# Optimization experiments

Measured on AMD Instinct MI355X. Metric: run time of the kernel, lower is better.

Reference implementation:

```python
import jax, jax.numpy as jnp
import numpy as np

NUM_HEADS = 8
WS = 7          # window size (hardcoded in source)
SR = 4          # sr_ratio
EPS = 1e-5


def _win_partition(t, ws, H, W):
    # t: [B, h, N, d] -> [B*h*nW, ws*ws, d]
    B, h, N, d = t.shape
    t = t.reshape(B * h, H // ws, ws, W // ws, ws, d)
    t = t.transpose(0, 1, 3, 2, 4, 5)
    return t.reshape(-1, ws * ws, d)


def _win_reverse(w, ws, H, W, h):
    # w: [B*h*nW, ws*ws, d] -> [B, H*W, h*d]
    d = w.shape[-1]
    Bh = w.shape[0] // ((H // ws) * (W // ws))
    x = w.reshape(Bh, H // ws, W // ws, ws, ws, d).transpose(0, 1, 3, 2, 4, 5)
    x = x.reshape(Bh // h, h, H, W, d).transpose(0, 2, 3, 1, 4)
    return x.reshape(Bh // h, H * W, h * d)


def setup_inputs() -> dict:
    key = jax.random.key(0)
    B, H, W, C = 32, 56, 56, 256
    N = H * W
    ks = jax.random.split(key, 10)
    s = lambda k, shp: jax.random.normal(k, shp, dtype=jnp.float32) * 0.02
    return {
        "x": jax.random.normal(ks[0], (B, N, C), dtype=jnp.float32),
        "lepe_lin_w": s(ks[1], (C, C)), "lepe_lin_b": jnp.zeros((C,), jnp.float32),
        "lepe_conv_w": s(ks[2], (3, 3, 1, C)), "lepe_conv_b": jnp.zeros((C,), jnp.float32),
        "sr_w": s(ks[3], (SR, SR, C, C)), "sr_b": jnp.zeros((C,), jnp.float32),
        "norm_g": jnp.ones((C,), jnp.float32), "norm_b": jnp.zeros((C,), jnp.float32),
        "q1_w": s(ks[4], (C, C // 2)), "kv1_w": s(ks[5], (C, C)),
        "q2_w": s(ks[6], (C, C // 2)), "kv2_w": s(ks[7], (C, C)),
        "proj_w": s(ks[8], (C, C)), "proj_b": jnp.zeros((C,), jnp.float32),
        "H": H, "W": W,
    }


def reference(x, lepe_lin_w, lepe_lin_b, lepe_conv_w, lepe_conv_b, sr_w, sr_b,
              norm_g, norm_b, q1_w, kv1_w, q2_w, kv2_w, proj_w, proj_b, H, W):
    B, N, C = x.shape
    h2 = NUM_HEADS // 2
    d = C // NUM_HEADS
    scale = d ** (-0.5)

    # lepe: linear -> depthwise 3x3 conv (NHWC) -> flatten back
    lep = (x @ lepe_lin_w + lepe_lin_b).reshape(B, H, W, C)
    lep = jax.lax.conv_general_dilated(
        lep, lepe_conv_w, window_strides=(1, 1), padding='SAME',
        dimension_numbers=('NHWC', 'HWIO', 'NHWC'), feature_group_count=C) + lepe_conv_b
    lepe = lep.reshape(B, N, C)

    # --- branch 1: global attention over sr-downsampled kv ---
    q1 = (x @ q1_w).reshape(B, N, h2, d).transpose(0, 2, 1, 3)         # [B,h2,N,d]
    img = x.reshape(B, H, W, C)
    x1_ = jax.lax.conv_general_dilated(
        img, sr_w, window_strides=(SR, SR), padding='VALID',
        dimension_numbers=('NHWC', 'HWIO', 'NHWC')) + sr_b              # [B,H/sr,W/sr,C]
    x1_ = x1_.reshape(B, -1, C)                                         # [B,N1,C]
    mu = jnp.mean(x1_, axis=-1, keepdims=True)
    var = jnp.mean(jnp.square(x1_ - mu), axis=-1, keepdims=True)
    x1_ = (x1_ - mu) * jax.lax.rsqrt(var + EPS) * norm_g + norm_b
    x1_ = jax.nn.gelu(x1_, approximate=False)
    kv1 = (x1_ @ kv1_w).reshape(B, -1, 2, h2, d).transpose(2, 0, 3, 1, 4)
    k1, v1 = kv1[0], kv1[1]                                             # [B,h2,N1,d]
    attn1 = jax.nn.softmax(jnp.einsum('bhnd,bhmd->bhnm', q1, k1) * scale, axis=-1)
    x1 = jnp.einsum('bhnm,bhmd->bhnd', attn1, v1)
    x1 = x1.transpose(0, 2, 1, 3).reshape(B, N, C // 2)

    # --- branch 2: 7x7 window attention ---
    q2 = (x @ q2_w).reshape(B, N, h2, d).transpose(0, 2, 1, 3)          # [B,h2,N,d]
    kv2 = (x @ kv2_w).reshape(B, -1, 2, h2, d).transpose(2, 0, 3, 1, 4)
    k2, v2 = kv2[0], kv2[1]
    q2w = _win_partition(q2, WS, H, W)                                  # [B*h2*nW,49,d]
    k2w = _win_partition(k2, WS, H, W)
    v2w = _win_partition(v2, WS, H, W)
    attn2 = jax.nn.softmax(jnp.einsum('wnd,wmd->wnm', q2w, k2w) * scale, axis=-1)
    x2w = jnp.einsum('wnm,wmd->wnd', attn2, v2w)
    x2 = _win_reverse(x2w, WS, H, W, h2)                                # [B,N,C/2]

    out = jnp.concatenate([x1, x2], axis=-1)
    out = (out + lepe) @ proj_w + proj_b
    return out
```

## Files before the change

kernel.cpp:

```cpp
#include <hip/hip_runtime.h>
#include <hip/hip_bf16.h>

typedef __hip_bfloat16 bf16;
typedef __attribute__((ext_vector_type(8))) short short8;
typedef __attribute__((ext_vector_type(4))) float floatx4;

__device__ __forceinline__ float toF(bf16 v){ return __bfloat162float(v); }
__device__ __forceinline__ float b2f(unsigned short u){
  return __uint_as_float(((unsigned int)u) << 16);
}
__device__ __forceinline__ unsigned short f2bu(float f){
  bf16 h = __float2bfloat16(f);
  return *(unsigned short*)&h;
}
__device__ __forceinline__ void storeT(bf16* p, float v){ *p = __float2bfloat16(v); }
__device__ __forceinline__ void storeT(float* p, float v){ *p = v; }

__device__ __forceinline__ void gl2l16(const void* g, void* l) {
  __builtin_amdgcn_global_load_lds(
      (const __attribute__((address_space(1))) unsigned int*)g,
      (__attribute__((address_space(3))) unsigned int*)l, 16, 0, 0);
}

__global__ __launch_bounds__(256) void cvt_x_kernel(
    const float* __restrict__ in, bf16* __restrict__ out) {
  size_t i4 = ((size_t)blockIdx.x * 256 + threadIdx.x) * 4;
  float4 v = *(const float4*)(in + i4);
  ushort4 o;
  o.x = f2bu(v.x); o.y = f2bu(v.y); o.z = f2bu(v.z); o.w = f2bu(v.w);
  *(ushort4*)(out + i4) = o;
}

__global__ __launch_bounds__(256) void prep_kernel(
    const float* __restrict__ sr_w, const float* __restrict__ lepe_w,
    const float* __restrict__ kv2_w, const float* __restrict__ q1_w,
    const float* __restrict__ q2_w, const float* __restrict__ kv1_w,
    const float* __restrict__ proj_w,
    bf16* __restrict__ wT_sr, bf16* __restrict__ wT_x,
    bf16* __restrict__ wT_kv1, bf16* __restrict__ wT_proj,
    int* __restrict__ srbase) {
  const int bid = blockIdx.x, tid = threadIdx.x;
  const float* src; bf16* dst; int K, N, idx;
  if (bid < 4096)      { src = sr_w;   dst = wT_sr;          K = 4096; N = 256; idx = bid * 256 + tid; }
  else if (bid < 4352) { src = lepe_w; dst = wT_x;           K = 256;  N = 256; idx = (bid - 4096) * 256 + tid; }
  else if (bid < 4608) { src = kv2_w;  dst = wT_x + 65536;   K = 256;  N = 256; idx = (bid - 4352) * 256 + tid; }
  else if (bid < 4736) { src = q1_w;   dst = wT_x + 131072;  K = 256;  N = 128; idx = (bid - 4608) * 256 + tid; }
  else if (bid < 4864) { src = q2_w;   dst = wT_x + 163840;  K = 256;  N = 128; idx = (bid - 4736) * 256 + tid; }
  else if (bid < 5120) { src = kv1_w;  dst = wT_kv1;         K = 256;  N = 256; idx = (bid - 4864) * 256 + tid; }
  else if (bid < 5376) { src = proj_w; dst = wT_proj;        K = 256;  N = 256; idx = (bid - 5120) * 256 + tid; }
  else {
    int t = (bid - 5376) * 256 + tid;
    if (t < 6272) {
      int b = t / 196, p = t - b * 196;
      int oy = p / 14, ox = p - oy * 14;
      srbase[t] = ((b * 56 + oy * 4) * 56 + ox * 4) * 256;
    }
    return;
  }
  int k = idx / N, n = idx - k * N;
  dst[(size_t)n * K + k] = __float2bfloat16(src[idx]);
}

template<typename OT>
__global__ __launch_bounds__(256) void gemm_mfma(
    const bf16* __restrict__ A, const bf16* __restrict__ BT,
    const float* __restrict__ bias, OT* __restrict__ C,
    int M, int K, int N) {
  __shared__ bf16 As[128 * 32];
  __shared__ bf16 Bs[128 * 32];
  const int tid = threadIdx.x;
  const int m0 = blockIdx.y * 128;
  const int n0 = blockIdx.x * 128;
  const int wave = tid >> 6, lane = tid & 63;
  const int wm = (wave >> 1) * 64, wn = (wave & 1) * 64;
  const int l15 = lane & 15, quad = lane >> 4;
  const int srow = lane >> 2, sseg = lane & 3;
  floatx4 zero = {0.f, 0.f, 0.f, 0.f};
  floatx4 acc[4][4];
#pragma unroll
  for (int i = 0; i < 4; i++)
#pragma unroll
    for (int j = 0; j < 4; j++) acc[i][j] = zero;

  for (int k0 = 0; k0 < K; k0 += 32) {
#pragma unroll
    for (int t = 0; t < 2; t++) {
      int rb = wave * 32 + t * 16;
      int r = rb + srow;
      gl2l16(A + (size_t)(m0 + r) * K + k0 + sseg * 8, &As[rb * 32]);
      gl2l16(BT + (size_t)(n0 + r) * K + k0 + sseg * 8, &Bs[rb * 32]);
    }
    __syncthreads();
    short8 af[4], bfr[4];
#pragma unroll
    for (int i = 0; i < 4; i++)
      af[i] = *(const short8*)&As[(wm + i * 16 + l15) * 32 + quad * 8];
#pragma unroll
    for (int j = 0; j < 4; j++)
      bfr[j] = *(const short8*)&Bs[(wn + j * 16 + l15) * 32 + quad * 8];
#pragma unroll
    for (int i = 0; i < 4; i++)
#pragma unroll
      for (int j = 0; j < 4; j++)
        acc[i][j] = __builtin_amdgcn_mfma_f32_16x16x32_bf16(af[i], bfr[j], acc[i][j], 0, 0, 0);
    __syncthreads();
  }
#pragma unroll
  for (int j = 0; j < 4; j++) {
    int n = n0 + wn + j * 16 + l15;
    float bv = bias ? bias[n] : 0.0f;
#pragma unroll
    for (int i = 0; i < 4; i++) {
      int m = m0 + wm + i * 16 + quad * 4;
#pragma unroll
      for (int r = 0; r < 4; r++)
        storeT(&C[(size_t)(m + r) * N + n], acc[i][j][r] + bv);
    }
  }
}

__global__ __launch_bounds__(256) void gemm_x3(
    const bf16* __restrict__ A, const bf16* __restrict__ BT,
    const float* __restrict__ lepe_b,
    bf16* __restrict__ L1, bf16* __restrict__ KV2, bf16* __restrict__ Q12) {
  __shared__ bf16 As[128 * 32];
  __shared__ bf16 Bs[128 * 32];
  const int sw = (blockIdx.x & 7) * 588 + (blockIdx.x >> 3);
  const int bx = sw % 6, by = sw / 6;
  const int m0 = by * 128;
  const int n0 = bx * 128;
  const int tid = threadIdx.x;
  const int wave = tid >> 6, lane = tid & 63;
  const int wm = (wave >> 1) * 64, wn = (wave & 1) * 64;
  const int l15 = lane & 15, quad = lane >> 4;
  const int srow = lane >> 2, sseg = lane & 3;
  floatx4 zero = {0.f, 0.f, 0.f, 0.f};
  floatx4 acc[4][4];
#pragma unroll
  for (int i = 0; i < 4; i++)
#pragma unroll
    for (int j = 0; j < 4; j++) acc[i][j] = zero;

  for (int k0 = 0; k0 < 256; k0 += 32) {
#pragma unroll
    for (int t = 0; t < 2; t++) {
      int rb = wave * 32 + t * 16;
      int r = rb + srow;
      gl2l16(A + (size_t)(m0 + r) * 256 + k0 + sseg * 8, &As[rb * 32]);
      gl2l16(BT + (size_t)(n0 + r) * 256 + k0 + sseg * 8, &Bs[rb * 32]);
    }
    __syncthreads();
    short8 af[4], bfr[4];
#pragma unroll
    for (int i = 0; i < 4; i++)
      af[i] = *(const short8*)&As[(wm + i * 16 + l15) * 32 + quad * 8];
#pragma unroll
    for (int j = 0; j < 4; j++)
      bfr[j] = *(const short8*)&Bs[(wn + j * 16 + l15) * 32 + quad * 8];
#pragma unroll
    for (int i = 0; i < 4; i++)
#pragma unroll
      for (int j = 0; j < 4; j++)
        acc[i][j] = __builtin_amdgcn_mfma_f32_16x16x32_bf16(af[i], bfr[j], acc[i][j], 0, 0, 0);
    __syncthreads();
  }
  const int segN = n0 >> 8;
  bf16* Cd = (segN == 0) ? L1 : (segN == 1) ? KV2 : Q12;
  const int nc0 = n0 & 255;
#pragma unroll
  for (int j = 0; j < 4; j++) {
    int nl = nc0 + wn + j * 16 + l15;
    float bv = (segN == 0) ? lepe_b[nl] : 0.0f;
#pragma unroll
    for (int i = 0; i < 4; i++) {
      int m = m0 + wm + i * 16 + quad * 4;
#pragma unroll
      for (int r = 0; r < 4; r++)
        Cd[(size_t)(m + r) * 256 + nl] = __float2bfloat16(acc[i][j][r] + bv);
    }
  }
}

__global__ __launch_bounds__(256) void gemm_sr(
    const bf16* __restrict__ X, const bf16* __restrict__ BT,
    const int* __restrict__ base, float* __restrict__ C) {
  __shared__ bf16 As[128 * 32];
  __shared__ bf16 Bs[128 * 32];
  const int tid = threadIdx.x;
  const int m0 = blockIdx.y * 128;
  const int n0 = blockIdx.x * 128;
  const int kz = blockIdx.z;
  const int wave = tid >> 6, lane = tid & 63;
  const int wm = (wave >> 1) * 64, wn = (wave & 1) * 64;
  const int l15 = lane & 15, quad = lane >> 4;
  const int srow = lane >> 2, sseg = lane & 3;
  const int mb0 = base[m0 + wave * 32 + srow];
  const int mb1 = base[m0 + wave * 32 + 16 + srow];
  floatx4 zero = {0.f, 0.f, 0.f, 0.f};
  floatx4 acc[4][4];
#pragma unroll
  for (int i = 0; i < 4; i++)
#pragma unroll
    for (int j = 0; j < 4; j++) acc[i][j] = zero;

  const int kbeg = kz * 512;
  for (int k0 = kbeg; k0 < kbeg + 512; k0 += 32) {
    int k = k0 + sseg * 8;
    int kp = k >> 8, c = k & 255;
    int off = ((kp >> 2) * 56 + (kp & 3)) * 256 + c;
#pragma unroll
    for (int t = 0; t < 2; t++) {
      int rb = wave * 32 + t * 16;
      gl2l16(X + (size_t)(t ? mb1 : mb0) + off, &As[rb * 32]);
      gl2l16(BT + (size_t)(n0 + rb + srow) * 4096 + k, &Bs[rb * 32]);
    }
    __syncthreads();
    short8 af[4], bfr[4];
#pragma unroll
    for (int i = 0; i < 4; i++)
      af[i] = *(const short8*)&As[(wm + i * 16 + l15) * 32 + quad * 8];
#pragma unroll
    for (int j = 0; j < 4; j++)
      bfr[j] = *(const short8*)&Bs[(wn + j * 16 + l15) * 32 + quad * 8];
#pragma unroll
    for (int i = 0; i < 4; i++)
#pragma unroll
      for (int j = 0; j < 4; j++)
        acc[i][j] = __builtin_amdgcn_mfma_f32_16x16x32_bf16(af[i], bfr[j], acc[i][j], 0, 0, 0);
    __syncthreads();
  }
  float* Cp = C + (size_t)kz * (6272 * 256);
#pragma unroll
  for (int j = 0; j < 4; j++) {
    int n = n0 + wn + j * 16 + l15;
#pragma unroll
    for (int i = 0; i < 4; i++) {
      int m = m0 + wm + i * 16 + quad * 4;
#pragma unroll
      for (int r = 0; r < 4; r++)
        Cp[(size_t)(m + r) * 256 + n] = acc[i][j][r];
    }
  }
}

__global__ __launch_bounds__(256) void gemm_proj_mfma(
    const bf16* __restrict__ X1, const bf16* __restrict__ X2,
    const bf16* __restrict__ L2, const bf16* __restrict__ BT,
    const float* __restrict__ bias, float* __restrict__ C) {
  __shared__ uint4 As[128 * 5];
  __shared__ bf16 Bs[128 * 32];
  const int sw = (blockIdx.x & 7) * 196 + (blockIdx.x >> 3);
  const int tid = threadIdx.x;
  const int m0 = (sw >> 1) * 128;
  const int n0 = (sw & 1) * 128;
  const int wave = tid >> 6, lane = tid & 63;
  const int wm = (wave >> 1) * 64, wn = (wave & 1) * 64;
  const int l15 = lane & 15, quad = lane >> 4;
  const int srow = lane >> 2, sseg = lane & 3;
  floatx4 zero = {0.f, 0.f, 0.f, 0.f};
  floatx4 acc[4][4];
#pragma unroll
  for (int i = 0; i < 4; i++)
#pragma unroll
    for (int j = 0; j < 4; j++) acc[i][j] = zero;

  for (int k0 = 0; k0 < 256; k0 += 32) {
#pragma unroll
    for (int t = 0; t < 2; t++) {
      int rb = wave * 32 + t * 16;
      gl2l16(BT + (size_t)(n0 + rb + srow) * 256 + k0 + sseg * 8, &Bs[rb * 32]);
    }
#pragma unroll
    for (int it = 0; it < 2; it++) {
      int id = it * 256 + tid;
      int row = id >> 2, seg = id & 3;
      int k = k0 + seg * 8;
      int mrow = m0 + row;
      const bf16* src = (k < 128) ? X1 + (size_t)mrow * 128 + k
                                  : X2 + (size_t)mrow * 128 + (k - 128);
      uint4 va = *(const uint4*)src;
      uint4 vl = *(const uint4*)(L2 + (size_t)mrow * 256 + k);
      const unsigned short* pa = (const unsigned short*)&va;
      const unsigned short* pl = (const unsigned short*)&vl;
      unsigned short ov[8];
#pragma unroll
      for (int e = 0; e < 8; e++) ov[e] = f2bu(b2f(pa[e]) + b2f(pl[e]));
      As[row * 5 + seg] = *(const uint4*)ov;
    }
    __syncthreads();
    short8 af[4], bfr[4];
#pragma unroll
    for (int i = 0; i < 4; i++)
      af[i] = *(const short8*)&As[(wm + i * 16 + l15) * 5 + quad];
#pragma unroll
    for (int j = 0; j < 4; j++)
      bfr[j] = *(const short8*)&Bs[(wn + j * 16 + l15) * 32 + quad * 8];
#pragma unroll
    for (int i = 0; i < 4; i++)
#pragma unroll
      for (int j = 0; j < 4; j++)
        acc[i][j] = __builtin_amdgcn_mfma_f32_16x16x32_bf16(af[i], bfr[j], acc[i][j], 0, 0, 0);
    __syncthreads();
  }
#pragma unroll
  for (int j = 0; j < 4; j++) {
    int n = n0 + wn + j * 16 + l15;
    float bv = bias[n];
#pragma unroll
    for (int i = 0; i < 4; i++) {
      int m = m0 + wm + i * 16 + quad * 4;
#pragma unroll
      for (int r = 0; r < 4; r++)
        C[(size_t)(m + r) * 256 + n] = acc[i][j][r] + bv;
    }
  }
}

__global__ __launch_bounds__(256) void dwconv8_kernel(
    const bf16* __restrict__ in, const float* __restrict__ w,
    const float* __restrict__ bias, bf16* __restrict__ out) {
  const int idx = blockIdx.x * 256 + threadIdx.x;
  const int c8 = (idx & 31) * 8;
  const int sp = idx >> 5;
  const int xx = sp % 56;
  const int yb = sp / 56;
  const int yy = yb % 56;
  const int b  = yb / 56;
  float4 bb0 = *(const float4*)&bias[c8];
  float4 bb1 = *(const float4*)&bias[c8 + 4];
  float acc[8] = {bb0.x, bb0.y, bb0.z, bb0.w, bb1.x, bb1.y, bb1.z, bb1.w};
#pragma unroll
  for (int dy = 0; dy < 3; dy++) {
    int y = yy + dy - 1;
    if ((unsigned)y >= 56u) continue;
#pragma unroll
    for (int dx = 0; dx < 3; dx++) {
      int x = xx + dx - 1;
      if ((unsigned)x >= 56u) continue;
      uint4 v = *(const uint4*)&in[((size_t)((b * 56 + y) * 56 + x)) * 256 + c8];
      const unsigned short* pv = (const unsigned short*)&v;
      float4 w0 = *(const float4*)&w[(dy * 3 + dx) * 256 + c8];
      float4 w1 = *(const float4*)&w[(dy * 3 + dx) * 256 + c8 + 4];
      float wf[8] = {w0.x, w0.y, w0.z, w0.w, w1.x, w1.y, w1.z, w1.w};
#pragma unroll
      for (int e = 0; e < 8; e++) acc[e] += b2f(pv[e]) * wf[e];
    }
  }
  unsigned short o[8];
#pragma unroll
  for (int e = 0; e < 8; e++) o[e] = f2bu(acc[e]);
  *(uint4*)&out[(size_t)sp * 256 + c8] = *(const uint4*)o;
}

__global__ __launch_bounds__(256) void ln_gelu_kernel(
    const float* __restrict__ in, const float* __restrict__ srb,
    const float* __restrict__ g, const float* __restrict__ bb,
    bf16* __restrict__ out) {
  const int tok = blockIdx.x;
  const int tid = threadIdx.x;
  float v = srb[tid];
  const float* p = in + (size_t)tok * 256 + tid;
#pragma unroll
  for (int c = 0; c < 8; c++) v += p[(size_t)c * 1605632];
  float s = v, s2 = v * v;
#pragma unroll
  for (int o = 32; o > 0; o >>= 1) {
    s += __shfl_down(s, o, 64);
    s2 += __shfl_down(s2, o, 64);
  }
  __shared__ float rs[4], rs2[4];
  int wid = tid >> 6, lane = tid & 63;
  if (lane == 0) { rs[wid] = s; rs2[wid] = s2; }
  __syncthreads();
  float tot = rs[0] + rs[1] + rs[2] + rs[3];
  float tot2 = rs2[0] + rs2[1] + rs2[2] + rs2[3];
  float mean = tot * (1.0f / 256.0f);
  float var = tot2 * (1.0f / 256.0f) - mean * mean;
  float y = (v - mean) * rsqrtf(var + 1e-5f) * g[tid] + bb[tid];
  out[(size_t)tok * 256 + tid] =
      __float2bfloat16(0.5f * y * (1.0f + erff(y * 0.70710678118654752f)));
}

__global__ __launch_bounds__(256) void attn1_mfma(
    const bf16* __restrict__ Q12, const float* __restrict__ KV,
    bf16* __restrict__ O) {
  __shared__ bf16 sk[224 * 32];
  __shared__ bf16 svT[32 * 232];
  __shared__ bf16 pbuf[4][64 * 32];
  const int b = blockIdx.z, h = blockIdx.y, chunk = blockIdx.x;
  const int tid = threadIdx.x;
  const int wave = tid >> 6, lane = tid & 63;
  const int l15 = lane & 15, quad = lane >> 4;
  for (int i = tid; i < 224 * 8; i += 256) {
    int m = i >> 3, c = i & 7;
    float4 kf = {0.f, 0.f, 0.f, 0.f}, vf = {0.f, 0.f, 0.f, 0.f};
    if (m < 196) {
      const float* p = KV + ((size_t)(b * 196 + m)) * 256 + h * 32 + c * 4;
      kf = *(const float4*)p;
      vf = *(const float4*)(p + 128);
    }
    ushort4 ko;
    ko.x = f2bu(kf.x); ko.y = f2bu(kf.y); ko.z = f2bu(kf.z); ko.w = f2bu(kf.w);
    *(ushort4*)&sk[m * 32 + c * 4] = ko;
    svT[(c * 4 + 0) * 232 + m] = __float2bfloat16(vf.x);
    svT[(c * 4 + 1) * 232 + m] = __float2bfloat16(vf.y);
    svT[(c * 4 + 2) * 232 + m] = __float2bfloat16(vf.z);
    svT[(c * 4 + 3) * 232 + m] = __float2bfloat16(vf.w);
  }
  __syncthreads();
  const int q0 = chunk * 256 + wave * 64;
  short8 aq[4];
#pragma unroll
  for (int i = 0; i < 4; i++) {
    int qr = q0 + i * 16 + l15; if (qr > 3135) qr = 3135;
    aq[i] = *(const short8*)(Q12 + ((size_t)(b * 3136 + qr)) * 256 + h * 32 + quad * 8);
  }
  const float scale = 0.17677669529663687f;
  floatx4 zero = {0.f, 0.f, 0.f, 0.f};
  floatx4 acc[4][2];
  float lsum[4][4];
#pragma unroll
  for (int i = 0; i < 4; i++) {
    acc[i][0] = zero; acc[i][1] = zero;
#pragma unroll
    for (int r = 0; r < 4; r++) lsum[i][r] = 0.f;
  }
  bf16* pw = pbuf[wave];
  for (int c = 0; c < 7; c++) {
    const int kv0 = c * 32;
    short8 bk[2];
#pragma unroll
    for (int n = 0; n < 2; n++)
      bk[n] = *(const short8*)&sk[(kv0 + n * 16 + l15) * 32 + quad * 8];
    floatx4 s[4][2];
#pragma unroll
    for (int i = 0; i < 4; i++)
#pragma unroll
      for (int n = 0; n < 2; n++)
        s[i][n] = __builtin_amdgcn_mfma_f32_16x16x32_bf16(aq[i], bk[n], zero, 0, 0, 0);
#pragma unroll
    for (int i = 0; i < 4; i++)
#pragma unroll
      for (int n = 0; n < 2; n++) {
        bool valid = (kv0 + n * 16 + l15) < 196;
#pragma unroll
        for (int r = 0; r < 4; r++) {
          float p = valid ? __expf(s[i][n][r] * scale) : 0.f;
          lsum[i][r] += p;
          pw[(i * 16 + quad * 4 + r) * 32 + n * 16 + l15] = __float2bfloat16(p);
        }
      }
    asm volatile("s_waitcnt lgkmcnt(0)" ::: "memory");
    short8 ap[4], bv[2];
#pragma unroll
    for (int i = 0; i < 4; i++)
      ap[i] = *(const short8*)&pw[(i * 16 + l15) * 32 + quad * 8];
#pragma unroll
    for (int n = 0; n < 2; n++)
      bv[n] = *(const short8*)&svT[(n * 16 + l15) * 232 + kv0 + quad * 8];
#pragma unroll
    for (int i = 0; i < 4; i++)
#pragma unroll
      for (int n = 0; n < 2; n++)
        acc[i][n] = __builtin_amdgcn_mfma_f32_16x16x32_bf16(ap[i], bv[n], acc[i][n], 0, 0, 0);
  }
#pragma unroll
  for (int i = 0; i < 4; i++)
#pragma unroll
    for (int r = 0; r < 4; r++) {
      float v = lsum[i][r];
      v += __shfl_xor(v, 1, 64);
      v += __shfl_xor(v, 2, 64);
      v += __shfl_xor(v, 4, 64);
      v += __shfl_xor(v, 8, 64);
      lsum[i][r] = 1.0f / v;
    }
#pragma unroll
  for (int i = 0; i < 4; i++)
#pragma unroll
    for (int r = 0; r < 4; r++) {
      int qr = q0 + i * 16 + quad * 4 + r;
      if (qr < 3136) {
        bf16* op = O + ((size_t)(b * 3136 + qr)) * 128 + h * 32;
        op[l15]      = __float2bfloat16(acc[i][0][r] * lsum[i][r]);
        op[16 + l15] = __float2bfloat16(acc[i][1][r] * lsum[i][r]);
      }
    }
}

__global__ __launch_bounds__(256) void attn2_mfma(
    const bf16* __restrict__ Q12, const bf16* __restrict__ KV2,
    bf16* __restrict__ O) {
  __shared__ bf16 sk[64 * 136];
  __shared__ bf16 pb[4][64 * 72];
  const int b = blockIdx.y;
  const int win = blockIdx.x;
  const int wy = win >> 3, wx = win & 7;
  const int tid = threadIdx.x;
  const int wave = tid >> 6, lane = tid & 63;
  const int l15 = lane & 15, quad = lane >> 4;
  const int h = wave;

  for (int i = tid; i < 49 * 16; i += 256) {
    int m = i >> 4, c = i & 15;
    int iy = m / 7, ix = m - iy * 7;
    int n = (wy * 7 + iy) * 56 + wx * 7 + ix;
    *(uint4*)&sk[m * 136 + c * 8] =
        *(const uint4*)&KV2[((size_t)(b * 3136 + n)) * 256 + c * 8];
  }

  short8 bvv[2][2];
#pragma unroll
  for (int ks = 0; ks < 2; ks++)
#pragma unroll
    for (int nt = 0; nt < 2; nt++)
#pragma unroll
      for (int e = 0; e < 8; e++) {
        int k = ks * 32 + quad * 8 + e; if (k > 48) k = 48;
        int iy = k / 7, ix = k - iy * 7;
        int n = (wy * 7 + iy) * 56 + wx * 7 + ix;
        bvv[ks][nt][e] = ((const short*)KV2)[((size_t)(b * 3136 + n)) * 256
                                             + 128 + h * 32 + nt * 16 + l15];
      }

  short8 aq[4];
#pragma unroll
  for (int i = 0; i < 4; i++) {
    int lq = i * 16 + l15; if (lq > 48) lq = 48;
    int iy = lq / 7, ix = lq - iy * 7;
    int n = (wy * 7 + iy) * 56 + wx * 7 + ix;
    aq[i] = *(const short8*)(Q12 + ((size_t)(b * 3136 + n)) * 256 + 128 + h * 32 + quad * 8);
  }
  __syncthreads();

  const float scale = 0.17677669529663687f;
  floatx4 zero = {0.f, 0.f, 0.f, 0.f};
  floatx4 acc[4][2];
  float lsum[4][4];
#pragma unroll
  for (int i = 0; i < 4; i++) {
    acc[i][0] = zero; acc[i][1] = zero;
#pragma unroll
    for (int r = 0; r < 4; r++) lsum[i][r] = 0.f;
  }
  bf16* pw = pb[wave];
#pragma unroll
  for (int c = 0; c < 2; c++) {
    const int kv0 = c * 32;
    short8 bk[2];
#pragma unroll
    for (int n = 0; n < 2; n++)
      bk[n] = *(const short8*)&sk[(kv0 + n * 16 + l15) * 136 + h * 32 + quad * 8];
    floatx4 s[4][2];
#pragma unroll
    for (int i = 0; i < 4; i++)
#pragma unroll
      for (int n = 0; n < 2; n++)
        s[i][n] = __builtin_amdgcn_mfma_f32_16x16x32_bf16(aq[i], bk[n], zero, 0, 0, 0);
#pragma unroll
    for (int i = 0; i < 4; i++)
#pragma unroll
      for (int n = 0; n < 2; n++) {
        bool valid = (kv0 + n * 16 + l15) < 49;
#pragma unroll
        for (int r = 0; r < 4; r++) {
          float p = valid ? __expf(s[i][n][r] * scale) : 0.f;
          lsum[i][r] += p;
          pw[(i * 16 + quad * 4 + r) * 72 + kv0 + n * 16 + l15] = __float2bfloat16(p);
        }
      }
  }
  asm volatile("s_waitcnt lgkmcnt(0)" ::: "memory");
#pragma unroll
  for (int ks = 0; ks < 2; ks++) {
    short8 ap[4];
#pragma unroll
    for (int i = 0; i < 4; i++)
      ap[i] = *(const short8*)&pw[(i * 16 + l15) * 72 + ks * 32 + quad * 8];
#pragma unroll
    for (int i = 0; i < 4; i++)
#pragma unroll
      for (int nt = 0; nt < 2; nt++)
        acc[i][nt] = __builtin_amdgcn_mfma_f32_16x16x32_bf16(ap[i], bvv[ks][nt], acc[i][nt], 0, 0, 0);
  }
#pragma unroll
  for (int i = 0; i < 4; i++)
#pragma unroll
    for (int r = 0; r < 4; r++) {
      float v = lsum[i][r];
      v += __shfl_xor(v, 1, 64);
      v += __shfl_xor(v, 2, 64);
      v += __shfl_xor(v, 4, 64);
      v += __shfl_xor(v, 8, 64);
      lsum[i][r] = 1.0f / v;
    }
#pragma unroll
  for (int i = 0; i < 4; i++)
#pragma unroll
    for (int r = 0; r < 4; r++) {
      int lq = i * 16 + quad * 4 + r;
      if (lq < 49) {
        int iy = lq / 7, ix = lq - iy * 7;
        int n = (wy * 7 + iy) * 56 + wx * 7 + ix;
        bf16* op = O + ((size_t)(b * 3136 + n)) * 128 + h * 32;
        op[l15]      = __float2bfloat16(acc[i][0][r] * lsum[i][r]);
        op[16 + l15] = __float2bfloat16(acc[i][1][r] * lsum[i][r]);
      }
    }
}

extern "C" void kernel_launch(void* const* d_in, const int* in_sizes, int n_in,
                              void* d_out, int out_size, void* d_ws, size_t ws_size,
                              hipStream_t stream) {
  const float* x           = (const float*)d_in[0];
  const float* lepe_lin_w  = (const float*)d_in[1];
  const float* lepe_lin_b  = (const float*)d_in[2];
  const float* lepe_conv_w = (const float*)d_in[3];
  const float* lepe_conv_b = (const float*)d_in[4];
  const float* sr_w        = (const float*)d_in[5];
  const float* sr_b        = (const float*)d_in[6];
  const float* norm_g      = (const float*)d_in[7];
  const float* norm_b      = (const float*)d_in[8];
  const float* q1_w        = (const float*)d_in[9];
  const float* kv1_w       = (const float*)d_in[10];
  const float* q2_w        = (const float*)d_in[11];
  const float* kv2_w       = (const float*)d_in[12];
  const float* proj_w      = (const float*)d_in[13];
  const float* proj_b      = (const float*)d_in[14];
  float* out = (float*)d_out;

  char* ws = (char*)d_ws;
  char* ob = (char*)d_out;
  const size_t szBNC = 100352ull * 256 * 2;
  const size_t szBNh = 100352ull * 128 * 2;
  bf16*  xb  = (bf16*)ob;
  bf16*  Q12 = (bf16*)(ob + szBNC);
  bf16*  L1  = (bf16*)ws;
  float* X1Ppart = (float*)ws;
  bf16*  X1N = (bf16*)ob;
  float* KV1 = (float*)(ob + 8388608);
  bf16*  X1  = (bf16*)ws;
  bf16*  L2  = (bf16*)(ws + szBNC);
  bf16*  X2  = (bf16*)(ws + 2 * szBNC);
  char*  wtb = ws + 2 * szBNC + szBNh;
  bf16* wT_x    = (bf16*)(wtb);
  bf16* wT_kv1  = (bf16*)(wtb + 393216);
  bf16* wT_proj = (bf16*)(wtb + 524288);
  bf16* wT_sr   = (bf16*)(wtb + 655360);
  int*  srbase  = (int*)(wtb + 655360 + 2097152);
  bf16* KV2     = (bf16*)(wtb + 655360 + 2097152 + 32768);

  cvt_x_kernel<<<25088, 256, 0, stream>>>(x, xb);
  prep_kernel<<<5401, 256, 0, stream>>>(
      sr_w, lepe_lin_w, kv2_w, q1_w, q2_w, kv1_w, proj_w,
      wT_sr, wT_x, wT_kv1, wT_proj, srbase);

  gemm_x3<<<4704, 256, 0, stream>>>(xb, wT_x, lepe_lin_b, L1, KV2, Q12);

  dwconv8_kernel<<<12544, 256, 0, stream>>>(L1, lepe_conv_w, lepe_conv_b, L2);

  attn2_mfma<<<dim3(64, 32), 256, 0, stream>>>(Q12, KV2, X2);

  gemm_sr<<<dim3(2, 49, 8), 256, 0, stream>>>(xb, wT_sr, srbase, X1Ppart);
  ln_gelu_kernel<<<6272, 256, 0, stream>>>(X1Ppart, sr_b, norm_g, norm_b, X1N);
  gemm_mfma<float><<<dim3(2, 49), 256, 0, stream>>>(
      X1N, wT_kv1, nullptr, KV1, 6272, 256, 256);
  attn1_mfma<<<dim3(13, 4, 32), 256, 0, stream>>>(Q12, KV1, X1);

  gemm_proj_mfma<<<1568, 256, 0, stream>>>(
      X1, X2, L2, wT_proj, proj_b, out);
}
```

Before: 536.6 us.

## Double-buffer LDS tiles in all MFMA GEMMs and vectorize output stores

Every MFMA GEMM kernel (x3, sr, kv1, proj) now keeps two LDS buffers and issues the global-to-LDS loads for the next K tile before computing on the current one, leaving one barrier per iteration. This hides global load latency behind MFMA work. The MFMA operands are swapped so each lane holds four consecutive output columns, which lets the epilogues write float4 or ushort4 vectors instead of scalar strided stores. The cost is double the shared memory per block, which may lower occupancy.

```diff
diff --git a/kernel.cpp b/kernel.cpp
--- a/kernel.cpp
+++ b/kernel.cpp
@@ -13,8 +13,6 @@
   bf16 h = __float2bfloat16(f);
   return *(unsigned short*)&h;
 }
-__device__ __forceinline__ void storeT(bf16* p, float v){ *p = __float2bfloat16(v); }
-__device__ __forceinline__ void storeT(float* p, float v){ *p = v; }
 
 __device__ __forceinline__ void gl2l16(const void* g, void* l) {
   __builtin_amdgcn_global_load_lds(
@@ -61,13 +59,11 @@
   dst[(size_t)n * K + k] = __float2bfloat16(src[idx]);
 }
 
-template<typename OT>
-__global__ __launch_bounds__(256) void gemm_mfma(
+__global__ __launch_bounds__(256) void gemm_mfma_f(
     const bf16* __restrict__ A, const bf16* __restrict__ BT,
-    const float* __restrict__ bias, OT* __restrict__ C,
-    int M, int K, int N) {
-  __shared__ bf16 As[128 * 32];
-  __shared__ bf16 Bs[128 * 32];
+    float* __restrict__ C, int K, int N) {
+  __shared__ bf16 As[2][128 * 32];
+  __shared__ bf16 Bs[2][128 * 32];
   const int tid = threadIdx.x;
   const int m0 = blockIdx.y * 128;
   const int n0 = blockIdx.x * 128;
@@ -75,6 +71,9 @@
   const int wm = (wave >> 1) * 64, wn = (wave & 1) * 64;
   const int l15 = lane & 15, quad = lane >> 4;
   const int srow = lane >> 2, sseg = lane & 3;
+  const bf16* aptr = A + (size_t)(m0 + wave * 32 + srow) * K + sseg * 8;
+  const bf16* bptr = BT + (size_t)(n0 + wave * 32 + srow) * K + sseg * 8;
+  const int rb = wave * 32;
   floatx4 zero = {0.f, 0.f, 0.f, 0.f};
   floatx4 acc[4][4];
 #pragma unroll
@@ -82,39 +81,44 @@
 #pragma unroll
     for (int j = 0; j < 4; j++) acc[i][j] = zero;
 
-  for (int k0 = 0; k0 < K; k0 += 32) {
-#pragma unroll
-    for (int t = 0; t < 2; t++) {
-      int rb = wave * 32 + t * 16;
-      int r = rb + srow;
-      gl2l16(A + (size_t)(m0 + r) * K + k0 + sseg * 8, &As[rb * 32]);
-      gl2l16(BT + (size_t)(n0 + r) * K + k0 + sseg * 8, &Bs[rb * 32]);
-    }
+  const int NT = K >> 5;
+  gl2l16(aptr, &As[0][rb * 32]);
+  gl2l16(aptr + (size_t)16 * K, &As[0][(rb + 16) * 32]);
+  gl2l16(bptr, &Bs[0][rb * 32]);
+  gl2l16(bptr + (size_t)16 * K, &Bs[0][(rb + 16) * 32]);
+  __syncthreads();
+  int cur = 0;
+  for (int t = 0; t < NT; t++) {
+    if (t + 1 < NT) {
+      int k0 = (t + 1) * 32;
+      gl2l16(aptr + k0, &As[cur ^ 1][rb * 32]);
+      gl2l16(aptr + (size_t)16 * K + k0, &As[cur ^ 1][(rb + 16) * 32]);
+      gl2l16(bptr + k0, &Bs[cur ^ 1][rb * 32]);
+      gl2l16(bptr + (size_t)16 * K + k0, &Bs[cur ^ 1][(rb + 16) * 32]);
+    }
+    short8 af[4], bfr[4];
+#pragma unroll
+    for (int i = 0; i < 4; i++)
+      af[i] = *(const short8*)&As[cur][(wm + i * 16 + l15) * 32 + quad * 8];
+#pragma unroll
+    for (int j = 0; j < 4; j++)
+      bfr[j] = *(const short8*)&Bs[cur][(wn + j * 16 + l15) * 32 + quad * 8];
+#pragma unroll
+    for (int i = 0; i < 4; i++)
+#pragma unroll
+      for (int j = 0; j < 4; j++)
+        acc[i][j] = __builtin_amdgcn_mfma_f32_16x16x32_bf16(bfr[j], af[i], acc[i][j], 0, 0, 0);
     __syncthreads();
-    short8 af[4], bfr[4];
-#pragma unroll
-    for (int i = 0; i < 4; i++)
-      af[i] = *(const short8*)&As[(wm + i * 16 + l15) * 32 + quad * 8];
-#pragma unroll
-    for (int j = 0; j < 4; j++)
-      bfr[j] = *(const short8*)&Bs[(wn + j * 16 + l15) * 32 + quad * 8];
-#pragma unroll
-    for (int i = 0; i < 4; i++)
-#pragma unroll
-      for (int j = 0; j < 4; j++)
-        acc[i][j] = __builtin_amdgcn_mfma_f32_16x16x32_bf16(af[i], bfr[j], acc[i][j], 0, 0, 0);
-    __syncthreads();
-  }
-#pragma unroll
-  for (int j = 0; j < 4; j++) {
-    int n = n0 + wn + j * 16 + l15;
-    float bv = bias ? bias[n] : 0.0f;
-#pragma unroll
-    for (int i = 0; i < 4; i++) {
-      int m = m0 + wm + i * 16 + quad * 4;
-#pragma unroll
-      for (int r = 0; r < 4; r++)
-        storeT(&C[(size_t)(m + r) * N + n], acc[i][j][r] + bv);
+    cur ^= 1;
+  }
+#pragma unroll
+  for (int i = 0; i < 4; i++) {
+    int m = m0 + wm + i * 16 + l15;
+#pragma unroll
+    for (int j = 0; j < 4; j++) {
+      int nb = n0 + wn + j * 16 + quad * 4;
+      float4 o = {acc[i][j][0], acc[i][j][1], acc[i][j][2], acc[i][j][3]};
+      *(float4*)&C[(size_t)m * N + nb] = o;
     }
   }
 }
@@ -123,8 +127,8 @@
     const bf16* __restrict__ A, const bf16* __restrict__ BT,
     const float* __restrict__ lepe_b,
     bf16* __restrict__ L1, bf16* __restrict__ KV2, bf16* __restrict__ Q12) {
-  __shared__ bf16 As[128 * 32];
-  __shared__ bf16 Bs[128 * 32];
+  __shared__ bf16 As[2][128 * 32];
+  __shared__ bf16 Bs[2][128 * 32];
   const int sw = (blockIdx.x & 7) * 588 + (blockIdx.x >> 3);
   const int bx = sw % 6, by = sw / 6;
   const int m0 = by * 128;
@@ -134,6 +138,9 @@
   const int wm = (wave >> 1) * 64, wn = (wave & 1) * 64;
   const int l15 = lane & 15, quad = lane >> 4;
   const int srow = lane >> 2, sseg = lane & 3;
+  const bf16* aptr = A + (size_t)(m0 + wave * 32 + srow) * 256 + sseg * 8;
+  const bf16* bptr = BT + (size_t)(n0 + wave * 32 + srow) * 256 + sseg * 8;
+  const int rb = wave * 32;
   floatx4 zero = {0.f, 0.f, 0.f, 0.f};
   floatx4 acc[4][4];
 #pragma unroll
@@ -141,42 +148,53 @@
 #pragma unroll
     for (int j = 0; j < 4; j++) acc[i][j] = zero;
 
-  for (int k0 = 0; k0 < 256; k0 += 32) {
-#pragma unroll
-    for (int t = 0; t < 2; t++) {
-      int rb = wave * 32 + t * 16;
-      int r = rb + srow;
-      gl2l16(A + (size_t)(m0 + r) * 256 + k0 + sseg * 8, &As[rb * 32]);
-      gl2l16(BT + (size_t)(n0 + r) * 256 + k0 + sseg * 8, &Bs[rb * 32]);
-    }
+  gl2l16(aptr, &As[0][rb * 32]);
+  gl2l16(aptr + 16 * 256, &As[0][(rb + 16) * 32]);
+  gl2l16(bptr, &Bs[0][rb * 32]);
+  gl2l16(bptr + 16 * 256, &Bs[0][(rb + 16) * 32]);
+  __syncthreads();
+  int cur = 0;
+#pragma unroll
+  for (int t = 0; t < 8; t++) {
+    if (t < 7) {
+      int k0 = (t + 1) * 32;
+      gl2l16(aptr + k0, &As[cur ^ 1][rb * 32]);
+      gl2l16(aptr + 16 * 256 + k0, &As[cur ^ 1][(rb + 16) * 32]);
+      gl2l16(bptr + k0, &Bs[cur ^ 1][rb * 32]);
+      gl2l16(bptr + 16 * 256 + k0, &Bs[cur ^ 1][(rb + 16) * 32]);
+    }
+    short8 af[4], bfr[4];
+#pragma unroll
+    for (int i = 0; i < 4; i++)
+      af[i] = *(const short8*)&As[cur][(wm + i * 16 + l15) * 32 + quad * 8];
+#pragma unroll
+    for (int j = 0; j < 4; j++)
+      bfr[j] = *(const short8*)&Bs[cur][(wn + j * 16 + l15) * 32 + quad * 8];
+#pragma unroll
+    for (int i = 0; i < 4; i++)
+#pragma unroll
+      for (int j = 0; j < 4; j++)
+        acc[i][j] = __builtin_amdgcn_mfma_f32_16x16x32_bf16(bfr[j], af[i], acc[i][j], 0, 0, 0);
     __syncthreads();
-    short8 af[4], bfr[4];
-#pragma unroll
-    for (int i = 0; i < 4; i++)
-      af[i] = *(const short8*)&As[(wm + i * 16 + l15) * 32 + quad * 8];
-#pragma unroll
-    for (int j = 0; j < 4; j++)
-      bfr[j] = *(const short8*)&Bs[(wn + j * 16 + l15) * 32 + quad * 8];
-#pragma unroll
-    for (int i = 0; i < 4; i++)
-#pragma unroll
-      for (int j = 0; j < 4; j++)
-        acc[i][j] = __builtin_amdgcn_mfma_f32_16x16x32_bf16(af[i], bfr[j], acc[i][j], 0, 0, 0);
-    __syncthreads();
+    cur ^= 1;
   }
   const int segN = n0 >> 8;
   bf16* Cd = (segN == 0) ? L1 : (segN == 1) ? KV2 : Q12;
   const int nc0 = n0 & 255;
 #pragma unroll
-  for (int j = 0; j < 4; j++) {
-    int nl = nc0 + wn + j * 16 + l15;
-    float bv = (segN == 0) ? lepe_b[nl] : 0.0f;
-#pragma unroll
-    for (int i = 0; i < 4; i++) {
-      int m = m0 + wm + i * 16 + quad * 4;
-#pragma unroll
-      for (int r = 0; r < 4; r++)
-        Cd[(size_t)(m + r) * 256 + nl] = __float2bfloat16(acc[i][j][r] + bv);
+  for (int i = 0; i < 4; i++) {
+    int m = m0 + wm + i * 16 + l15;
+#pragma unroll
+    for (int j = 0; j < 4; j++) {
+      int nb = nc0 + wn + j * 16 + quad * 4;
+      float4 bv = {0.f, 0.f, 0.f, 0.f};
+      if (segN == 0) bv = *(const float4*)&lepe_b[nb];
+      ushort4 o;
+      o.x = f2bu(acc[i][j][0] + bv.x);
+      o.y = f2bu(acc[i][j][1] + bv.y);
+      o.z = f2bu(acc[i][j][2] + bv.z);
+      o.w = f2bu(acc[i][j][3] + bv.w);
+      *(ushort4*)&Cd[(size_t)m * 256 + nb] = o;
     }
   }
 }
@@ -184,8 +202,8 @@
 __global__ __launch_bounds__(256) void gemm_sr(
     const bf16* __restrict__ X, const bf16* __restrict__ BT,
     const int* __restrict__ base, float* __restrict__ C) {
-  __shared__ bf16 As[128 * 32];
-  __shared__ bf16 Bs[128 * 32];
+  __shared__ bf16 As[2][128 * 32];
+  __shared__ bf16 Bs[2][128 * 32];
   const int tid = threadIdx.x;
   const int m0 = blockIdx.y * 128;
   const int n0 = blockIdx.x * 128;
@@ -196,6 +214,9 @@
   const int srow = lane >> 2, sseg = lane & 3;
   const int mb0 = base[m0 + wave * 32 + srow];
   const int mb1 = base[m0 + wave * 32 + 16 + srow];
+  const bf16* bptr = BT + (size_t)(n0 + wave * 32 + srow) * 4096 + sseg * 8;
+  const int rb = wave * 32;
+  const int kbeg = kz * 512;
   floatx4 zero = {0.f, 0.f, 0.f, 0.f};
   floatx4 acc[4][4];
 #pragma unroll
@@ -203,42 +224,51 @@
 #pragma unroll
     for (int j = 0; j < 4; j++) acc[i][j] = zero;
 
-  const int kbeg = kz * 512;
-  for (int k0 = kbeg; k0 < kbeg + 512; k0 += 32) {
-    int k = k0 + sseg * 8;
+  {
+    int k = kbeg + sseg * 8;
     int kp = k >> 8, c = k & 255;
     int off = ((kp >> 2) * 56 + (kp & 3)) * 256 + c;
-#pragma unroll
-    for (int t = 0; t < 2; t++) {
-      int rb = wave * 32 + t * 16;
-      gl2l16(X + (size_t)(t ? mb1 : mb0) + off, &As[rb * 32]);
-      gl2l16(BT + (size_t)(n0 + rb + srow) * 4096 + k, &Bs[rb * 32]);
-    }
+    gl2l16(X + (size_t)mb0 + off, &As[0][rb * 32]);
+    gl2l16(X + (size_t)mb1 + off, &As[0][(rb + 16) * 32]);
+    gl2l16(bptr + kbeg, &Bs[0][rb * 32]);
+    gl2l16(bptr + 16 * 4096 + kbeg, &Bs[0][(rb + 16) * 32]);
+  }
+  __syncthreads();
+  int cur = 0;
+  for (int t = 0; t < 16; t++) {
+    if (t < 15) {
+      int k = kbeg + (t + 1) * 32 + sseg * 8;
+      int kp = k >> 8, c = k & 255;
+      int off = ((kp >> 2) * 56 + (kp & 3)) * 256 + c;
+      gl2l16(X + (size_t)mb0 + off, &As[cur ^ 1][rb * 32]);
+      gl2l16(X + (size_t)mb1 + off, &As[cur ^ 1][(rb + 16) * 32]);
+      gl2l16(bptr + kbeg + (t + 1) * 32, &Bs[cur ^ 1][rb * 32]);
+      gl2l16(bptr + 16 * 4096 + kbeg + (t + 1) * 32, &Bs[cur ^ 1][(rb + 16) * 32]);
+    }
+    short8 af[4], bfr[4];
+#pragma unroll
+    for (int i = 0; i < 4; i++)
+      af[i] = *(const short8*)&As[cur][(wm + i * 16 + l15) * 32 + quad * 8];
+#pragma unroll
+    for (int j = 0; j < 4; j++)
+      bfr[j] = *(const short8*)&Bs[cur][(wn + j * 16 + l15) * 32 + quad * 8];
+#pragma unroll
+    for (int i = 0; i < 4; i++)
+#pragma unroll
+      for (int j = 0; j < 4; j++)
+        acc[i][j] = __builtin_amdgcn_mfma_f32_16x16x32_bf16(bfr[j], af[i], acc[i][j], 0, 0, 0);
     __syncthreads();
-    short8 af[4], bfr[4];
-#pragma unroll
-    for (int i = 0; i < 4; i++)
-      af[i] = *(const short8*)&As[(wm + i * 16 + l15) * 32 + quad * 8];
-#pragma unroll
-    for (int j = 0; j < 4; j++)
-      bfr[j] = *(const short8*)&Bs[(wn + j * 16 + l15) * 32 + quad * 8];
-#pragma unroll
-    for (int i = 0; i < 4; i++)
-#pragma unroll
-      for (int j = 0; j < 4; j++)
-        acc[i][j] = __builtin_amdgcn_mfma_f32_16x16x32_bf16(af[i], bfr[j], acc[i][j], 0, 0, 0);
-    __syncthreads();
+    cur ^= 1;
   }
   float* Cp = C + (size_t)kz * (6272 * 256);
 #pragma unroll
-  for (int j = 0; j < 4; j++) {
-    int n = n0 + wn + j * 16 + l15;
-#pragma unroll
-    for (int i = 0; i < 4; i++) {
-      int m = m0 + wm + i * 16 + quad * 4;
-#pragma unroll
-      for (int r = 0; r < 4; r++)
-        Cp[(size_t)(m + r) * 256 + n] = acc[i][j][r];
+  for (int i = 0; i < 4; i++) {
+    int m = m0 + wm + i * 16 + l15;
+#pragma unroll
+    for (int j = 0; j < 4; j++) {
+      int nb = n0 + wn + j * 16 + quad * 4;
+      float4 o = {acc[i][j][0], acc[i][j][1], acc[i][j][2], acc[i][j][3]};
+      *(float4*)&Cp[(size_t)m * 256 + nb] = o;
     }
   }
 }
@@ -247,8 +277,8 @@
     const bf16* __restrict__ X1, const bf16* __restrict__ X2,
     const bf16* __restrict__ L2, const bf16* __restrict__ BT,
     const float* __restrict__ bias, float* __restrict__ C) {
-  __shared__ uint4 As[128 * 5];
-  __shared__ bf16 Bs[128 * 32];
+  __shared__ uint4 As[2][128 * 5];
+  __shared__ bf16 Bs[2][128 * 32];
   const int sw = (blockIdx.x & 7) * 196 + (blockIdx.x >> 3);
   const int tid = threadIdx.x;
   const int m0 = (sw >> 1) * 128;
@@ -257,6 +287,9 @@
   const int wm = (wave >> 1) * 64, wn = (wave & 1) * 64;
   const int l15 = lane & 15, quad = lane >> 4;
   const int srow = lane >> 2, sseg = lane & 3;
+  const bf16* bptr = BT + (size_t)(n0 + wave * 32 + srow) * 256 + sseg * 8;
+  const int rb = wave * 32;
+  const int row0 = tid >> 2, row1 = 64 + (tid >> 2), segA = tid & 3;
   floatx4 zero = {0.f, 0.f, 0.f, 0.f};
   floatx4 acc[4][4];
 #pragma unroll
@@ -264,54 +297,90 @@
 #pragma unroll
     for (int j = 0; j < 4; j++) acc[i][j] = zero;
 
-  for (int k0 = 0; k0 < 256; k0 += 32) {
-#pragma unroll
-    for (int t = 0; t < 2; t++) {
-      int rb = wave * 32 + t * 16;
-      gl2l16(BT + (size_t)(n0 + rb + srow) * 256 + k0 + sseg * 8, &Bs[rb * 32]);
-    }
-#pragma unroll
-    for (int it = 0; it < 2; it++) {
-      int id = it * 256 + tid;
-      int row = id >> 2, seg = id & 3;
-      int k = k0 + seg * 8;
-      int mrow = m0 + row;
-      const bf16* src = (k < 128) ? X1 + (size_t)mrow * 128 + k
-                                  : X2 + (size_t)mrow * 128 + (k - 128);
-      uint4 va = *(const uint4*)src;
-      uint4 vl = *(const uint4*)(L2 + (size_t)mrow * 256 + k);
-      const unsigned short* pa = (const unsigned short*)&va;
-      const unsigned short* pl = (const unsigned short*)&vl;
-      unsigned short ov[8];
-#pragma unroll
-      for (int e = 0; e < 8; e++) ov[e] = f2bu(b2f(pa[e]) + b2f(pl[e]));
-      As[row * 5 + seg] = *(const uint4*)ov;
+  uint4 va0, va1, vl0, vl1;
+  {
+    int k = segA * 8;
+    const bf16* s0 = (k < 128) ? X1 + (size_t)(m0 + row0) * 128 + k
+                               : X2 + (size_t)(m0 + row0) * 128 + (k - 128);
+    const bf16* s1 = (k < 128) ? X1 + (size_t)(m0 + row1) * 128 + k
+                               : X2 + (size_t)(m0 + row1) * 128 + (k - 128);
+    va0 = *(const uint4*)s0; va1 = *(const uint4*)s1;
+    vl0 = *(const uint4*)(L2 + (size_t)(m0 + row0) * 256 + k);
+    vl1 = *(const uint4*)(L2 + (size_t)(m0 + row1) * 256 + k);
+  }
+  gl2l16(bptr, &Bs[0][rb * 32]);
+  gl2l16(bptr + 16 * 256, &Bs[0][(rb + 16) * 32]);
+  {
+    unsigned short o0[8], o1[8];
+    const unsigned short* pa0 = (const unsigned short*)&va0;
+    const unsigned short* pl0 = (const unsigned short*)&vl0;
+    const unsigned short* pa1 = (const unsigned short*)&va1;
+    const unsigned short* pl1 = (const unsigned short*)&vl1;
+#pragma unroll
+    for (int e = 0; e < 8; e++) {
+      o0[e] = f2bu(b2f(pa0[e]) + b2f(pl0[e]));
+      o1[e] = f2bu(b2f(pa1[e]) + b2f(pl1[e]));
+    }
+    As[0][row0 * 5 + segA] = *(const uint4*)o0;
+    As[0][row1 * 5 + segA] = *(const uint4*)o1;
+  }
+  __syncthreads();
+  int cur = 0;
+#pragma unroll
+  for (int t = 0; t < 8; t++) {
+    uint4 nva0, nva1, nvl0, nvl1;
+    if (t < 7) {
+      int k0 = (t + 1) * 32;
+      gl2l16(bptr + k0, &Bs[cur ^ 1][rb * 32]);
+      gl2l16(bptr + 16 * 256 + k0, &Bs[cur ^ 1][(rb + 16) * 32]);
+      int k = k0 + segA * 8;
+      const bf16* s0 = (k < 128) ? X1 + (size_t)(m0 + row0) * 128 + k
+                                 : X2 + (size_t)(m0 + row0) * 128 + (k - 128);
+      const bf16* s1 = (k < 128) ? X1 + (size_t)(m0 + row1) * 128 + k
+                                 : X2 + (size_t)(m0 + row1) * 128 + (k - 128);
+      nva0 = *(const uint4*)s0; nva1 = *(const uint4*)s1;
+      nvl0 = *(const uint4*)(L2 + (size_t)(m0 + row0) * 256 + k);
+      nvl1 = *(const uint4*)(L2 + (size_t)(m0 + row1) * 256 + k);
+    }
+    short8 af[4], bfr[4];
+#pragma unroll
+    for (int i = 0; i < 4; i++)
+      af[i] = *(const short8*)&As[cur][(wm + i * 16 + l15) * 5 + quad];
+#pragma unroll
+    for (int j = 0; j < 4; j++)
+      bfr[j] = *(const short8*)&Bs[cur][(wn + j * 16 + l15) * 32 + quad * 8];
+#pragma unroll
+    for (int i = 0; i < 4; i++)
+#pragma unroll
+      for (int j = 0; j < 4; j++)
+        acc[i][j] = __builtin_amdgcn_mfma_f32_16x16x32_bf16(bfr[j], af[i], acc[i][j], 0, 0, 0);
+    if (t < 7) {
+      unsigned short o0[8], o1[8];
+      const unsigned short* pa0 = (const unsigned short*)&nva0;
+      const unsigned short* pl0 = (const unsigned short*)&nvl0;
+      const unsigned short* pa1 = (const unsigned short*)&nva1;
+      const unsigned short* pl1 = (const unsigned short*)&nvl1;
+#pragma unroll
+      for (int e = 0; e < 8; e++) {
+        o0[e] = f2bu(b2f(pa0[e]) + b2f(pl0[e]));
+        o1[e] = f2bu(b2f(pa1[e]) + b2f(pl1[e]));
+      }
+      As[cur ^ 1][row0 * 5 + segA] = *(const uint4*)o0;
+      As[cur ^ 1][row1 * 5 + segA] = *(const uint4*)o1;
     }
     __syncthreads();
-    short8 af[4], bfr[4];
-#pragma unroll
-    for (int i = 0; i < 4; i++)
-      af[i] = *(const short8*)&As[(wm + i * 16 + l15) * 5 + quad];
-#pragma unroll
-    for (int j = 0; j < 4; j++)
-      bfr[j] = *(const short8*)&Bs[(wn + j * 16 + l15) * 32 + quad * 8];
-#pragma unroll
-    for (int i = 0; i < 4; i++)
-#pragma unroll
-      for (int j = 0; j < 4; j++)
-        acc[i][j] = __builtin_amdgcn_mfma_f32_16x16x32_bf16(af[i], bfr[j], acc[i][j], 0, 0, 0);
-    __syncthreads();
-  }
-#pragma unroll
-  for (int j = 0; j < 4; j++) {
-    int n = n0 + wn + j * 16 + l15;
-    float bv = bias[n];
-#pragma unroll
-    for (int i = 0; i < 4; i++) {
-      int m = m0 + wm + i * 16 + quad * 4;
-#pragma unroll
-      for (int r = 0; r < 4; r++)
-        C[(size_t)(m + r) * 256 + n] = acc[i][j][r] + bv;
+    cur ^= 1;
+  }
+#pragma unroll
+  for (int i = 0; i < 4; i++) {
+    int m = m0 + wm + i * 16 + l15;
+#pragma unroll
+    for (int j = 0; j < 4; j++) {
+      int nb = n0 + wn + j * 16 + quad * 4;
+      float4 bv = *(const float4*)&bias[nb];
+      float4 o = {acc[i][j][0] + bv.x, acc[i][j][1] + bv.y,
+                  acc[i][j][2] + bv.z, acc[i][j][3] + bv.w};
+      *(float4*)&C[(size_t)m * 256 + nb] = o;
     }
   }
 }
@@ -663,8 +732,7 @@
 
   gemm_sr<<<dim3(2, 49, 8), 256, 0, stream>>>(xb, wT_sr, srbase, X1Ppart);
   ln_gelu_kernel<<<6272, 256, 0, stream>>>(X1Ppart, sr_b, norm_g, norm_b, X1N);
-  gemm_mfma<float><<<dim3(2, 49), 256, 0, stream>>>(
-      X1N, wT_kv1, nullptr, KV1, 6272, 256, 256);
+  gemm_mfma_f<<<dim3(2, 49), 256, 0, stream>>>(X1N, wT_kv1, KV1, 256, 256);
   attn1_mfma<<<dim3(13, 4, 32), 256, 0, stream>>>(Q12, KV1, X1);
 
   gemm_proj_mfma<<<1568, 256, 0, stream>>>(
```

After: 536.5 us. About the same (-0.0%).
